# Performance work log

Hardware: AMD Instinct MI355X
Metric: run time of the kernel (lower is better)

Reference implementation:

```python
import jax, jax.numpy as jnp
import numpy as np

B, T, DIM, H, DH, DT = 2, 2048, 1024, 16, 64, 32
Q_TEMP, K_TEMP = 1.0, 1.0
EPS = float(np.finfo(np.float32).eps)  # torch RMSNorm default eps for fp32
INV_SQRT_DH = 1.0 / np.sqrt(DH)


def _get_time(length, head_time_delta, time_angles, with_time_delta):
    # [T,1,1] positions, optionally offset per head -> [T,H,1]
    pos = jnp.arange(length, dtype=jnp.float32)[:, None, None]
    if with_time_delta:
        pos = pos + head_time_delta[None, :, None]          # [T,H,1]
    else:
        pos = jnp.broadcast_to(pos, (length, H, 1))          # [T,H,1]
    ang = pos * time_angles                                  # [T,H,Dt]
    c, s = jnp.cos(ang), jnp.sin(ang)
    return jnp.concatenate([c + s, c - s], axis=-1) * INV_SQRT_DH  # [T,H,2Dt]


def setup_inputs() -> dict:
    key = jax.random.key(0)
    ks = jax.random.split(key, 6)
    sc = 0.02
    states = jax.random.normal(ks[0], (B, T, DIM), jnp.float32)
    attention_mask = jnp.ones((B, T), jnp.int32)
    ln_w = jnp.ones((DIM,), jnp.float32)
    time_angles = 10000.0 ** (-1.0 / jnp.arange(1, DT + 1, dtype=jnp.float32))
    head_time_delta = jax.random.uniform(ks[1], (H,), jnp.float32)
    Wq = jax.random.normal(ks[2], (H * DH, DIM), jnp.float32) * sc
    q_bias = jnp.zeros((H * DH,), jnp.float32)
    Wk = jax.random.normal(ks[3], (H * DH, DIM), jnp.float32) * sc
    bk = jnp.zeros((H * DH,), jnp.float32)
    Wv = jax.random.normal(ks[4], (H * DH, DIM), jnp.float32) * sc
    bv = jnp.zeros((H * DH,), jnp.float32)
    Wo = jax.random.normal(ks[5], (DIM, H * DH), jnp.float32) * sc
    bo = jnp.zeros((DIM,), jnp.float32)
    return dict(states=states, attention_mask=attention_mask, ln_w=ln_w,
                time_angles=time_angles, head_time_delta=head_time_delta,
                Wq=Wq, q_bias=q_bias, Wk=Wk, bk=bk, Wv=Wv, bv=bv, Wo=Wo, bo=bo)


def reference(states, attention_mask, ln_w, time_angles, head_time_delta,
              Wq, q_bias, Wk, bk, Wv, bv, Wo, bo):
    # RMSNorm
    x = states * jax.lax.rsqrt(jnp.mean(states * states, axis=-1, keepdims=True) + EPS) * ln_w
    m = attention_mask.astype(x.dtype)[:, :, None, None]   # [B,T,1,1]

    # Q path -> q_attentioned [B,T,T,H]
    q = (x @ Wq.T - jnp.exp(q_bias)).reshape(B, T, H, DH)
    q_sm = jax.nn.softmax(q / Q_TEMP * m, axis=-1)
    t_q = _get_time(T, head_time_delta, time_angles, True)   # [T,H,2Dt]
    t_k = _get_time(T, head_time_delta, time_angles, False)  # [T,H,2Dt]
    q_timed = jnp.sum(q_sm, axis=-1, keepdims=True) * t_q    # [B,T,H,2Dt]
    q_att = jnp.einsum('bthd,lhd->btlh', q_timed, t_k)       # [B,T,T,H]

    # KV path
    k = (x @ Wk.T + bk).reshape(B, T, H, DH)
    k_sm = jax.nn.softmax(k / K_TEMP * m, axis=-1)
    v = (x @ Wv.T + bv).reshape(B, T, H, DH)
    kv = k_sm * v                                            # [B,T,H,Dh]

    loading = jnp.einsum('btlh,blhd->bthd', q_att, kv)       # [B,T,H,Dh]
    return loading.reshape(B, T, DIM) @ Wo.T + bo
```

## Files before the change

### kernel.cpp

```cpp
#include <hip/hip_runtime.h>
#include <math.h>

#define T_ 2048
#define H_ 16

typedef __attribute__((ext_vector_type(8))) short bfx8;
typedef __attribute__((ext_vector_type(4))) float f32x4;

__device__ __forceinline__ short f2bf(float f) {
  union { float f; unsigned u; } x; x.f = f;
  unsigned r = (x.u + 0x7FFFu + ((x.u >> 16) & 1u)) >> 16;
  return (short)r;
}
__device__ __forceinline__ float bf2f(short s) {
  union { unsigned u; float f; } x;
  x.u = ((unsigned)(unsigned short)s) << 16;
  return x.f;
}

#define GLD_LDS(g, l) \
  __builtin_amdgcn_global_load_lds( \
      (const __attribute__((address_space(1))) void*)(g), \
      (__attribute__((address_space(3))) void*)(l), 16, 0, 0)

__global__ __launch_bounds__(256) void prep_kernel(
    const float* __restrict__ Wk, const float* __restrict__ Wv,
    const float* __restrict__ Wo, const float* __restrict__ angles,
    const float* __restrict__ states, const float* __restrict__ ln_w,
    short* __restrict__ Wkb, short* __restrict__ Wvb, short* __restrict__ Wob,
    short* __restrict__ xb, short* __restrict__ Cb, short* __restrict__ tkT,
    float* __restrict__ MtH) {
  const int blk = blockIdx.x;
  if (blk < 3072) {
    const int i = blk * 256 + threadIdx.x;
    const int which = i >> 18;
    const int idx = i & 262143;
    const float* s = (which == 0) ? Wk : (which == 1) ? Wv : Wo;
    short* d = (which == 0) ? Wkb : (which == 1) ? Wvb : Wob;
    const float4 v = ((const float4*)s)[idx];
    short4 r;
    r.x = f2bf(v.x); r.y = f2bf(v.y); r.z = f2bf(v.z); r.w = f2bf(v.w);
    ((short4*)d)[idx] = r;
  } else if (blk < 7168) {
    const int row = blk - 3072;
    const int tid = threadIdx.x;
    const float4 v = ((const float4*)(states + (size_t)row * 1024))[tid];
    float ss = v.x * v.x + v.y * v.y + v.z * v.z + v.w * v.w;
#pragma unroll
    for (int off = 32; off >= 1; off >>= 1) ss += __shfl_xor(ss, off);
    __shared__ float red[4];
    if ((tid & 63) == 0) red[tid >> 6] = ss;
    __syncthreads();
    const float tot = red[0] + red[1] + red[2] + red[3];
    const float scale = rsqrtf(tot * (1.0f / 1024.0f) + 1.1920928955078125e-07f);
    const float4 w = ((const float4*)ln_w)[tid];
    short4 o;
    o.x = f2bf(v.x * scale * w.x);
    o.y = f2bf(v.y * scale * w.y);
    o.z = f2bf(v.z * scale * w.z);
    o.w = f2bf(v.w * scale * w.w);
    ((short4*)(xb + (size_t)row * 1024))[tid] = o;
  } else if (blk < 7424) {
    const int gid = (blk - 7168) * 256 + threadIdx.x;
    const int j = gid & 31;
    const int t = gid >> 5;
    float s, c;
    sincosf((float)t * angles[j], &s, &c);
    Cb[(size_t)t * 64 + j] = f2bf(0.125f * c);
    Cb[(size_t)t * 64 + 32 + j] = f2bf(0.125f * s);
  } else if (blk < 7456) {
    const int gid = (blk - 7424) * 256 + threadIdx.x;
    const int tc = gid & 255;
    const int j = gid >> 8;
    const float th = angles[j];
    short lo[8], hi[8];
#pragma unroll
    for (int r = 0; r < 8; ++r) {
      float s, c;
      sincosf((float)(tc * 8 + r) * th, &s, &c);
      lo[r] = f2bf((c + s) * 0.125f);
      hi[r] = f2bf((c - s) * 0.125f);
    }
    short* base = tkT + (size_t)j * 2048 + tc * 8;
    *(short4*)(base) = *(short4*)&lo[0];
    *(short4*)(base + 4) = *(short4*)&lo[4];
    short* base2 = tkT + (size_t)(32 + j) * 2048 + tc * 8;
    *(short4*)(base2) = *(short4*)&hi[0];
    *(short4*)(base2 + 4) = *(short4*)&hi[4];
  } else {
    const int gid = (blk - 7456) * 256 + threadIdx.x;
    ((float4*)MtH)[gid] = make_float4(0.f, 0.f, 0.f, 0.f);
  }
}

__global__ __launch_bounds__(1024, 8) void kvgemm_kernel(
    const short* __restrict__ xb, const short* __restrict__ Wkb,
    const short* __restrict__ Wvb, const float* __restrict__ bk,
    const float* __restrict__ bv, const int* __restrict__ mask,
    const short* __restrict__ tkT, float* __restrict__ Mt) {
  __shared__ short smem[32768];
  short(*Vs)[64] = (short(*)[64])smem;
  short(*kvS)[132] = (short(*)[132])(smem + 8192);

  const int row0 = blockIdx.x * 128;
  const int h = blockIdx.y;
  const int t = threadIdx.x;
  const int lane = t & 63;
  const int wv = t >> 6;
  const bool isV = wv >= 8;
  const int wrow = (wv & 7) * 16;
  const int lrow = lane & 15;

  const int srow8 = t >> 3;
  const int kslotS = (t & 7) ^ (srow8 & 7);
  const short* gaS = xb + (size_t)(row0 + srow8) * 1024 + kslotS * 8;
  const short* gbS = isV ? Wvb + (size_t)(h * 64 + srow8 - 64) * 1024 + kslotS * 8
                         : Wkb + (size_t)(h * 64 + srow8) * 1024 + kslotS * 8;
  short* laS = smem + srow8 * 64 + (t & 7) * 8;
  short* lbS = isV ? smem + 12288 + (srow8 - 64) * 64 + (t & 7) * 8
                   : smem + 8192 + srow8 * 64 + (t & 7) * 8;
  const int bOff = isV ? 12288 : 8192;

#define STAGE(B, K)                        \
  do {                                     \
    GLD_LDS(gaS + (K), laS + (B) * 16384); \
    GLD_LDS(gbS + (K), lbS + (B) * 16384); \
  } while (0)

#define COMPUTE(B)                                                            \
  do {                                                                        \
    const short(*As_)[64] = (const short(*)[64])(smem + (B) * 16384);         \
    const short(*Bs_)[64] = (const short(*)[64])(smem + (B) * 16384 + bOff);  \
    _Pragma("unroll")                                                         \
    for (int kk = 0; kk < 2; ++kk) {                                          \
      const int pcol = ((kk * 4 + (lane >> 4)) ^ (lrow & 7)) * 8;             \
      const bfx8 af = *(const bfx8*)&As_[wrow + lrow][pcol];                  \
      bfx8 bf_[4];                                                            \
      _Pragma("unroll")                                                       \
      for (int j = 0; j < 4; ++j)                                             \
        bf_[j] = *(const bfx8*)&Bs_[j * 16 + lrow][pcol];                     \
      _Pragma("unroll")                                                       \
      for (int j = 0; j < 4; ++j)                                             \
        acc[j] = __builtin_amdgcn_mfma_f32_16x16x32_bf16(af, bf_[j], acc[j],  \
                                                         0, 0, 0);            \
    }                                                                         \
  } while (0)

  f32x4 acc[4] = {};
  STAGE(0, 0);
  __syncthreads();
  for (int k0 = 0; k0 < 1024; k0 += 128) {
    STAGE(1, k0 + 64);
    COMPUTE(0);
    __syncthreads();
    if (k0 + 128 < 1024) STAGE(0, k0 + 128);
    COMPUTE(1);
    __syncthreads();
  }
#undef STAGE
#undef COMPUTE

  const int rq = (lane >> 4) * 4;
  if (isV) {
#pragma unroll
    for (int j = 0; j < 4; ++j) {
      const float bb = bv[h * 64 + j * 16 + lrow];
#pragma unroll
      for (int rr = 0; rr < 4; ++rr)
        Vs[wrow + rq + rr][j * 16 + lrow] = f2bf(acc[j][rr] + bb);
    }
  }
  __syncthreads();
  if (!isV) {
    float bkc[4];
#pragma unroll
    for (int j = 0; j < 4; ++j) bkc[j] = bk[h * 64 + j * 16 + lrow];
    const int rowg0 = row0 + wrow + rq;
#pragma unroll
    for (int rr = 0; rr < 4; ++rr) {
      const float m = (float)mask[rowg0 + rr];
      float kf[4];
#pragma unroll
      for (int j = 0; j < 4; ++j) kf[j] = (acc[j][rr] + bkc[j]) * m;
      float mx = fmaxf(fmaxf(kf[0], kf[1]), fmaxf(kf[2], kf[3]));
#pragma unroll
      for (int off = 8; off >= 1; off >>= 1) mx = fmaxf(mx, __shfl_xor(mx, off));
      float s = 0.0f;
#pragma unroll
      for (int j = 0; j < 4; ++j) { kf[j] = expf(kf[j] - mx); s += kf[j]; }
#pragma unroll
      for (int off = 8; off >= 1; off >>= 1) s += __shfl_xor(s, off);
      const float inv = 1.0f / s;
#pragma unroll
      for (int j = 0; j < 4; ++j)
        acc[j][rr] = kf[j] * inv * bf2f(Vs[wrow + rq + rr][j * 16 + lrow]);
    }
#pragma unroll
    for (int j = 0; j < 4; ++j) {
      const int d = j * 16 + lrow;
      short4 o;
      o.x = f2bf(acc[j][0]); o.y = f2bf(acc[j][1]);
      o.z = f2bf(acc[j][2]); o.w = f2bf(acc[j][3]);
      *(short4*)&kvS[d][wrow + rq] = o;
    }
  }
  __syncthreads();
  if (wv < 4) {
    const int bb = row0 >> 11;
    const int tb = row0 & 2047;
    const short* tkb = tkT + (size_t)(wv * 16 + lrow) * 2048 + tb;
    const int kg = (lane >> 4) * 8;
    f32x4 macc[4] = {};
#pragma unroll
    for (int kc = 0; kc < 4; ++kc) {
      const bfx8 af = *(const bfx8*)(tkb + kc * 32 + kg);
#pragma unroll
      for (int j = 0; j < 4; ++j) {
        const bfx8 bf_ = *(const bfx8*)&kvS[j * 16 + lrow][kc * 32 + kg];
        macc[j] = __builtin_amdgcn_mfma_f32_16x16x32_bf16(af, bf_, macc[j], 0, 0, 0);
      }
    }
    float* Mb = Mt + (size_t)(bb * 16 + h) * 4096;
#pragma unroll
    for (int j = 0; j < 4; ++j) {
      const int d = j * 16 + lrow;
#pragma unroll
      for (int rr = 0; rr < 4; ++rr) {
        const int e = wv * 16 + rq + rr;
        atomicAdd(&Mb[(size_t)e * 64 + d], macc[j][rr]);
      }
    }
  }
}

__global__ __launch_bounds__(256) void foldhgemm_kernel(
    const short* __restrict__ Wob, const float* __restrict__ Mt,
    const float* __restrict__ angles, const float* __restrict__ delta,
    float* __restrict__ H) {
  const int bid = blockIdx.x;
  const int t = threadIdx.x;
  const int lane = t & 63;
  const int w = t >> 6;
  const int lrow = lane & 15;
  const int kg = (lane >> 4) * 8;
  const int h2 = bid & 7;
  const int ot = (bid >> 3) & 15;
  const int b = bid >> 7;
  const int orow = ot * 64 + w * 16 + lrow;
  float p[2][2], q[2][2];
#pragma unroll
  for (int hh = 0; hh < 2; ++hh) {
    const float dl = delta[h2 * 2 + hh];
#pragma unroll
    for (int aa = 0; aa < 2; ++aa) {
      float s, c;
      sincosf(dl * angles[aa * 16 + lrow], &s, &c);
      p[hh][aa] = c + s;
      q[hh][aa] = c - s;
    }
  }
  f32x4 acc[4] = {};
#pragma unroll
  for (int ks = 0; ks < 4; ++ks) {
    const int hh = ks >> 1;
    const int h = h2 * 2 + hh;
    const int d0 = (ks & 1) * 32 + kg;
    const float* Mthb = Mt + (size_t)(b * 16 + h) * 4096;
    const bfx8 af = *(const bfx8*)(Wob + (size_t)orow * 1024 + h * 64 + d0);
    float m0a[8], m1a[8], m0b[8], m1b[8];
    *(float4*)&m0a[0] = *(const float4*)(Mthb + lrow * 64 + d0);
    *(float4*)&m0a[4] = *(const float4*)(Mthb + lrow * 64 + d0 + 4);
    *(float4*)&m1a[0] = *(const float4*)(Mthb + (32 + lrow) * 64 + d0);
    *(float4*)&m1a[4] = *(const float4*)(Mthb + (32 + lrow) * 64 + d0 + 4);
    *(float4*)&m0b[0] = *(const float4*)(Mthb + (16 + lrow) * 64 + d0);
    *(float4*)&m0b[4] = *(const float4*)(Mthb + (16 + lrow) * 64 + d0 + 4);
    *(float4*)&m1b[0] = *(const float4*)(Mthb + (48 + lrow) * 64 + d0);
    *(float4*)&m1b[4] = *(const float4*)(Mthb + (48 + lrow) * 64 + d0 + 4);
    bfx8 bf0, bf1, bf2, bf3;
#pragma unroll
    for (int e = 0; e < 8; ++e) {
      bf0[e] = f2bf(p[hh][0] * m0a[e] + q[hh][0] * m1a[e]);
      bf1[e] = f2bf(p[hh][1] * m0b[e] + q[hh][1] * m1b[e]);
      bf2[e] = f2bf(q[hh][0] * m0a[e] - p[hh][0] * m1a[e]);
      bf3[e] = f2bf(q[hh][1] * m0b[e] - p[hh][1] * m1b[e]);
    }
    acc[0] = __builtin_amdgcn_mfma_f32_16x16x32_bf16(af, bf0, acc[0], 0, 0, 0);
    acc[1] = __builtin_amdgcn_mfma_f32_16x16x32_bf16(af, bf1, acc[1], 0, 0, 0);
    acc[2] = __builtin_amdgcn_mfma_f32_16x16x32_bf16(af, bf2, acc[2], 0, 0, 0);
    acc[3] = __builtin_amdgcn_mfma_f32_16x16x32_bf16(af, bf3, acc[3], 0, 0, 0);
  }
  float* Hb = H + (size_t)b * 65536;
  const int rq = (lane >> 4) * 4;
#pragma unroll
  for (int j = 0; j < 4; ++j) {
    const int kap = j * 16 + lrow;
#pragma unroll
    for (int rr = 0; rr < 4; ++rr) {
      const int o = ot * 64 + w * 16 + rq + rr;
      atomicAdd(&Hb[(size_t)o * 64 + kap], acc[j][rr]);
    }
  }
}

__global__ __launch_bounds__(256) void ofinal_kernel(
    const short* __restrict__ Cb, const float* __restrict__ H,
    const float* __restrict__ bo, float* __restrict__ out) {
  const int col0 = blockIdx.x * 128;
  const int row0 = blockIdx.y * 128;
  const int b = blockIdx.z;
  float* C = out + (size_t)b * 2097152;
  const float* Hb = H + (size_t)b * 65536;
  const int t = threadIdx.x;
  const int lane = t & 63;
  const int wv = t >> 6;
  const int wm = (wv & 1) * 64, wn = (wv >> 1) * 64;
  const int lrow = lane & 15;
  const int kg = (lane >> 4) * 8;
  f32x4 acc[4][4] = {};
#pragma unroll
  for (int k0 = 0; k0 < 64; k0 += 32) {
    bfx8 af[4], bf_[4];
#pragma unroll
    for (int i = 0; i < 4; ++i)
      af[i] = *(const bfx8*)(Cb + (size_t)(row0 + wm + i * 16 + lrow) * 64 + k0 + kg);
#pragma unroll
    for (int j = 0; j < 4; ++j) {
      const float* hp = Hb + (size_t)(col0 + wn + j * 16 + lrow) * 64 + k0 + kg;
      const float4 h0 = *(const float4*)hp;
      const float4 h1 = *(const float4*)(hp + 4);
      bfx8 bb;
      bb[0] = f2bf(h0.x); bb[1] = f2bf(h0.y); bb[2] = f2bf(h0.z); bb[3] = f2bf(h0.w);
      bb[4] = f2bf(h1.x); bb[5] = f2bf(h1.y); bb[6] = f2bf(h1.z); bb[7] = f2bf(h1.w);
      bf_[j] = bb;
    }
#pragma unroll
    for (int i = 0; i < 4; ++i)
#pragma unroll
      for (int j = 0; j < 4; ++j)
        acc[i][j] = __builtin_amdgcn_mfma_f32_16x16x32_bf16(af[i], bf_[j], acc[i][j], 0, 0, 0);
  }
  const int rq = (lane >> 4) * 4;
#pragma unroll
  for (int j = 0; j < 4; ++j) {
    const int c = col0 + wn + j * 16 + lrow;
    const float bb = bo[c];
#pragma unroll
    for (int i = 0; i < 4; ++i) {
      const int r = row0 + wm + i * 16 + rq;
#pragma unroll
      for (int rr = 0; rr < 4; ++rr)
        C[(size_t)(r + rr) * 1024 + c] = acc[i][j][rr] + bb;
    }
  }
}

extern "C" void kernel_launch(void* const* d_in, const int* in_sizes, int n_in,
                              void* d_out, int out_size, void* d_ws, size_t ws_size,
                              hipStream_t stream) {
  (void)in_sizes; (void)n_in; (void)out_size; (void)ws_size;
  const float* states = (const float*)d_in[0];
  const int* mask = (const int*)d_in[1];
  const float* ln_w = (const float*)d_in[2];
  const float* angles = (const float*)d_in[3];
  const float* delta = (const float*)d_in[4];
  const float* Wk = (const float*)d_in[7];
  const float* bk = (const float*)d_in[8];
  const float* Wv = (const float*)d_in[9];
  const float* bv = (const float*)d_in[10];
  const float* Wo = (const float*)d_in[11];
  const float* bo = (const float*)d_in[12];
  float* out = (float*)d_out;

  char* W = (char*)d_ws;
  short* xb  = (short*)(W);
  short* Wkb = (short*)(W + (8u << 20));
  short* Wvb = (short*)(W + (10u << 20));
  short* Wob = (short*)(W + (12u << 20));
  short* Cb  = (short*)(W + (14u << 20));
  short* tkT = (short*)(W + (14u << 20) + (256u << 10));
  float* Mt  = (float*)(W + (15u << 20));
  float* H   = (float*)(W + (15u << 20) + (512u << 10));

  prep_kernel<<<7712, 256, 0, stream>>>(Wk, Wv, Wo, angles, states, ln_w,
                                        Wkb, Wvb, Wob, xb, Cb, tkT, Mt);
  kvgemm_kernel<<<dim3(32, 16), 1024, 0, stream>>>(xb, Wkb, Wvb, bk, bv, mask,
                                                   tkT, Mt);
  foldhgemm_kernel<<<256, 256, 0, stream>>>(Wob, Mt, angles, delta, H);
  ofinal_kernel<<<dim3(8, 16, 2), 256, 0, stream>>>(Cb, H, bo, out);
}
```

Before: 142.4 us.

## Halve kvgemm block to 512 threads with 32-row per-wave tiles

The K/V projection kernel now runs with 8 waves instead of 16, and each wave computes a 32x64 output tile (two A fragments against four B fragments) instead of 16x64. Each thread issues four global-to-LDS loads per stage instead of two to cover the same 128-row A tile and both weight tiles. The aim is more MFMA work per LDS B-fragment read and less barrier overhead per block. The cost is more accumulator registers per thread and fewer waves to hide memory latency.

```diff
diff --git a/kernel.cpp b/kernel.cpp
--- a/kernel.cpp
+++ b/kernel.cpp
@@ -93,7 +93,7 @@
   }
 }
 
-__global__ __launch_bounds__(1024, 8) void kvgemm_kernel(
+__global__ __launch_bounds__(512, 4) void kvgemm_kernel(
     const short* __restrict__ xb, const short* __restrict__ Wkb,
     const short* __restrict__ Wvb, const float* __restrict__ bk,
     const float* __restrict__ bv, const int* __restrict__ mask,
@@ -107,24 +107,26 @@
   const int t = threadIdx.x;
   const int lane = t & 63;
   const int wv = t >> 6;
-  const bool isV = wv >= 8;
-  const int wrow = (wv & 7) * 16;
+  const bool isV = wv >= 4;
+  const int wrow = (wv & 3) * 32;
   const int lrow = lane & 15;
 
   const int srow8 = t >> 3;
   const int kslotS = (t & 7) ^ (srow8 & 7);
   const short* gaS = xb + (size_t)(row0 + srow8) * 1024 + kslotS * 8;
-  const short* gbS = isV ? Wvb + (size_t)(h * 64 + srow8 - 64) * 1024 + kslotS * 8
-                         : Wkb + (size_t)(h * 64 + srow8) * 1024 + kslotS * 8;
+  const short* gkS = Wkb + (size_t)(h * 64 + srow8) * 1024 + kslotS * 8;
+  const short* gvS = Wvb + (size_t)(h * 64 + srow8) * 1024 + kslotS * 8;
   short* laS = smem + srow8 * 64 + (t & 7) * 8;
-  short* lbS = isV ? smem + 12288 + (srow8 - 64) * 64 + (t & 7) * 8
-                   : smem + 8192 + srow8 * 64 + (t & 7) * 8;
+  short* lkS = smem + 8192 + srow8 * 64 + (t & 7) * 8;
+  short* lvS = smem + 12288 + srow8 * 64 + (t & 7) * 8;
   const int bOff = isV ? 12288 : 8192;
 
-#define STAGE(B, K)                        \
-  do {                                     \
-    GLD_LDS(gaS + (K), laS + (B) * 16384); \
-    GLD_LDS(gbS + (K), lbS + (B) * 16384); \
+#define STAGE(B, K)                                   \
+  do {                                                \
+    GLD_LDS(gaS + (K), laS + (B) * 16384);            \
+    GLD_LDS(gaS + 64 * 1024 + (K), laS + 4096 + (B) * 16384); \
+    GLD_LDS(gkS + (K), lkS + (B) * 16384);            \
+    GLD_LDS(gvS + (K), lvS + (B) * 16384);            \
   } while (0)
 
 #define COMPUTE(B)                                                            \
@@ -134,19 +136,24 @@
     _Pragma("unroll")                                                         \
     for (int kk = 0; kk < 2; ++kk) {                                          \
       const int pcol = ((kk * 4 + (lane >> 4)) ^ (lrow & 7)) * 8;             \
-      const bfx8 af = *(const bfx8*)&As_[wrow + lrow][pcol];                  \
-      bfx8 bf_[4];                                                            \
+      bfx8 af[2], bf_[4];                                                     \
+      _Pragma("unroll")                                                       \
+      for (int i = 0; i < 2; ++i)                                             \
+        af[i] = *(const bfx8*)&As_[wrow + i * 16 + lrow][pcol];               \
       _Pragma("unroll")                                                       \
       for (int j = 0; j < 4; ++j)                                             \
         bf_[j] = *(const bfx8*)&Bs_[j * 16 + lrow][pcol];                     \
       _Pragma("unroll")                                                       \
-      for (int j = 0; j < 4; ++j)                                             \
-        acc[j] = __builtin_amdgcn_mfma_f32_16x16x32_bf16(af, bf_[j], acc[j],  \
-                                                         0, 0, 0);            \
+      for (int i = 0; i < 2; ++i)                                             \
+        _Pragma("unroll")                                                     \
+        for (int j = 0; j < 4; ++j)                                           \
+          acc[i][j] = __builtin_amdgcn_mfma_f32_16x16x32_bf16(af[i], bf_[j],  \
+                                                              acc[i][j],     \
+                                                              0, 0, 0);       \
     }                                                                         \
   } while (0)
 
-  f32x4 acc[4] = {};
+  f32x4 acc[2][4] = {};
   STAGE(0, 0);
   __syncthreads();
   for (int k0 = 0; k0 < 1024; k0 += 128) {
@@ -166,8 +173,10 @@
     for (int j = 0; j < 4; ++j) {
       const float bb = bv[h * 64 + j * 16 + lrow];
 #pragma unroll
-      for (int rr = 0; rr < 4; ++rr)
-        Vs[wrow + rq + rr][j * 16 + lrow] = f2bf(acc[j][rr] + bb);
+      for (int i = 0; i < 2; ++i)
+#pragma unroll
+        for (int rr = 0; rr < 4; ++rr)
+          Vs[wrow + rq + i * 16 + rr][j * 16 + lrow] = f2bf(acc[i][j][rr] + bb);
     }
   }
   __syncthreads();
@@ -177,31 +186,38 @@
     for (int j = 0; j < 4; ++j) bkc[j] = bk[h * 64 + j * 16 + lrow];
     const int rowg0 = row0 + wrow + rq;
 #pragma unroll
-    for (int rr = 0; rr < 4; ++rr) {
-      const float m = (float)mask[rowg0 + rr];
-      float kf[4];
-#pragma unroll
-      for (int j = 0; j < 4; ++j) kf[j] = (acc[j][rr] + bkc[j]) * m;
-      float mx = fmaxf(fmaxf(kf[0], kf[1]), fmaxf(kf[2], kf[3]));
-#pragma unroll
-      for (int off = 8; off >= 1; off >>= 1) mx = fmaxf(mx, __shfl_xor(mx, off));
-      float s = 0.0f;
-#pragma unroll
-      for (int j = 0; j < 4; ++j) { kf[j] = expf(kf[j] - mx); s += kf[j]; }
-#pragma unroll
-      for (int off = 8; off >= 1; off >>= 1) s += __shfl_xor(s, off);
-      const float inv = 1.0f / s;
-#pragma unroll
-      for (int j = 0; j < 4; ++j)
-        acc[j][rr] = kf[j] * inv * bf2f(Vs[wrow + rq + rr][j * 16 + lrow]);
+    for (int i = 0; i < 2; ++i) {
+#pragma unroll
+      for (int rr = 0; rr < 4; ++rr) {
+        const float m = (float)mask[rowg0 + i * 16 + rr];
+        float kf[4];
+#pragma unroll
+        for (int j = 0; j < 4; ++j) kf[j] = (acc[i][j][rr] + bkc[j]) * m;
+        float mx = fmaxf(fmaxf(kf[0], kf[1]), fmaxf(kf[2], kf[3]));
+#pragma unroll
+        for (int off = 8; off >= 1; off >>= 1) mx = fmaxf(mx, __shfl_xor(mx, off));
+        float s = 0.0f;
+#pragma unroll
+        for (int j = 0; j < 4; ++j) { kf[j] = expf(kf[j] - mx); s += kf[j]; }
+#pragma unroll
+        for (int off = 8; off >= 1; off >>= 1) s += __shfl_xor(s, off);
+        const float inv = 1.0f / s;
+#pragma unroll
+        for (int j = 0; j < 4; ++j)
+          acc[i][j][rr] = kf[j] * inv *
+                          bf2f(Vs[wrow + rq + i * 16 + rr][j * 16 + lrow]);
+      }
     }
 #pragma unroll
     for (int j = 0; j < 4; ++j) {
       const int d = j * 16 + lrow;
-      short4 o;
-      o.x = f2bf(acc[j][0]); o.y = f2bf(acc[j][1]);
-      o.z = f2bf(acc[j][2]); o.w = f2bf(acc[j][3]);
-      *(short4*)&kvS[d][wrow + rq] = o;
+#pragma unroll
+      for (int i = 0; i < 2; ++i) {
+        short4 o;
+        o.x = f2bf(acc[i][j][0]); o.y = f2bf(acc[i][j][1]);
+        o.z = f2bf(acc[i][j][2]); o.w = f2bf(acc[i][j][3]);
+        *(short4*)&kvS[d][wrow + rq + i * 16] = o;
+      }
     }
   }
   __syncthreads();
@@ -383,8 +399,8 @@
 
   prep_kernel<<<7712, 256, 0, stream>>>(Wk, Wv, Wo, angles, states, ln_w,
                                         Wkb, Wvb, Wob, xb, Cb, tkT, Mt);
-  kvgemm_kernel<<<dim3(32, 16), 1024, 0, stream>>>(xb, Wkb, Wvb, bk, bv, mask,
-                                                   tkT, Mt);
+  kvgemm_kernel<<<dim3(32, 16), 512, 0, stream>>>(xb, Wkb, Wvb, bk, bv, mask,
+                                                  tkT, Mt);
   foldhgemm_kernel<<<256, 256, 0, stream>>>(Wob, Mt, angles, delta, H);
   ofinal_kernel<<<dim3(8, 16, 2), 256, 0, stream>>>(Cb, H, bo, out);
 }
```

Result: no change. 143.2 us (+0.6%).
